# Optimization experiments

Hardware: AMD Instinct MI355X
Metric: run time of the kernel (lower is better)

Reference implementation:

```python
import jax, jax.numpy as jnp
import numpy as np
from jax import lax

B, T, D, H = 32, 512, 1024, 1024


def setup_inputs() -> dict:
    key = jax.random.key(0)
    ks = jax.random.split(key, 6)
    inp = jax.random.normal(ks[0], (B, T, D), jnp.float32)
    attention_mask = jnp.ones((B, T), jnp.float32)
    nonzero_index = jax.random.randint(ks[1], (B, 1), 0, T)
    # Stacked gate weights, gate order (i, f, g, o); equivalent to 8 separate Linears.
    W_x = jax.random.normal(ks[2], (D, 4 * H), jnp.float32) * 0.02
    W_h = jax.random.normal(ks[3], (H, 4 * H), jnp.float32) * 0.02
    b_x = jax.random.normal(ks[4], (4 * H,), jnp.float32) * 0.02
    b_h = jax.random.normal(ks[5], (4 * H,), jnp.float32) * 0.02
    return {"input": inp, "attention_mask": attention_mask, "nonzero_index": nonzero_index,
            "W_x": W_x, "W_h": W_h, "b_x": b_x, "b_h": b_h}


def reference(input, attention_mask, nonzero_index, W_x, W_h, b_x, b_h):
    # Precompute all input-side gate projections in one big matmul: [B,T,4H]
    x_gates = jnp.einsum('btd,dg->btg', input, W_x) + b_x + b_h

    def step(carry, xg):
        h, c = carry                       # [B,H] each
        g = xg + h @ W_h                   # [B,4H]
        i, f, gg, o = jnp.split(g, 4, axis=-1)
        i = jax.nn.sigmoid(i)
        f = jax.nn.sigmoid(f)
        gg = jnp.tanh(gg)
        o = jax.nn.sigmoid(o)
        c = f * c + i * gg
        h = o * jnp.tanh(c)
        return (h, c), (h, c)

    h0 = jnp.zeros((B, H), x_gates.dtype)
    c0 = jnp.zeros((B, H), x_gates.dtype)
    _, (hs, cs) = lax.scan(step, (h0, c0), jnp.swapaxes(x_gates, 0, 1))  # [T,B,H]
    hts = jnp.swapaxes(hs, 0, 1)  # [B,T,H]
    cts = jnp.swapaxes(cs, 0, 1)
    # cls token gathered BEFORE masking (matches original order)
    cls_token = jnp.take_along_axis(hts, nonzero_index[:, :, None], axis=1)[:, 0, :]
    hts = hts * attention_mask[:, :, None]
    cts = cts * attention_mask[:, :, None]
    return (hts, hts, cts, cls_token)
```

## Files before the change

kernel.cpp:

```cpp
#include <hip/hip_runtime.h>
#include <stdint.h>


typedef _Float16 f16;
typedef __attribute__((ext_vector_type(8))) _Float16 f16x8;
typedef __attribute__((ext_vector_type(4))) float f32x4;

#define NG 2
#define BPG 128
#define NW 8

__device__ __forceinline__ float sigm(float v){ return 1.f/(1.f+__expf(-v)); }
__device__ __forceinline__ float tanh_(float v){ return 2.f/(1.f+__expf(-2.f*v)) - 1.f; }

__global__ __launch_bounds__(512, 2) void lstm_kernel(
    const float* __restrict__ xin, const float* __restrict__ amask,
    const int* __restrict__ nzidx, const float* __restrict__ Wx,
    const float* __restrict__ Wh, const float* __restrict__ bx,
    const float* __restrict__ bh, float* __restrict__ out,
    uint32_t* __restrict__ ws)
{
  __shared__ __align__(16) f16 Wl[128][64][8];
  __shared__ __align__(16) float pl[NW][2][64][4];
  __shared__ __align__(16) f16 hstage[16][8];

  const int tid  = threadIdx.x;
  const int lane = tid & 63;
  const int wid  = tid >> 6;
  const int r    = blockIdx.x & 127;
  const int G    = blockIdx.x >> 7;
  const int hbase = r * 8;

  uint32_t* flags = ws + (size_t)G * BPG;
  uint64_t* hb64 = (uint64_t*)(ws + 2 * BPG);

  for (int f = wid; f < 128; f += NW) {
    const int side = f >> 6, kf = (f >> 1) & 31, nt = f & 1;
    const int c16 = lane & 15, kslot = lane >> 4;
    const int g = nt * 2 + (c16 >> 3);
    const int gcol = g * 1024 + hbase + (c16 & 7);
    const int k0 = kf * 32 + kslot * 8;
    const float* Wsrc = side ? Wh : Wx;
    f16x8 v;
#pragma unroll
    for (int e = 0; e < 8; ++e) v[e] = (f16)Wsrc[(size_t)(k0 + e) * 4096 + gcol];
    *(f16x8*)&Wl[f][lane][0] = v;
  }
  const int b  = tid >> 3;
  const int hc = tid & 7;
  const int b_glob = G * 16 + b;
  float bias[4] = {0.f, 0.f, 0.f, 0.f};
  float cval = 0.f;
  int myidx = -1;
  if (tid < 128) {
#pragma unroll
    for (int g = 0; g < 4; ++g) {
      const int gcol = g * 1024 + hbase + hc;
      bias[g] = bx[gcol] + bh[gcol];
    }
    myidx = nzidx[b_glob];
  }
  __syncthreads();

  bool gave_up = false;
#pragma unroll 1
  for (int t = 0; t < 512; ++t) {
    f32x4 acc0 = {0.f,0.f,0.f,0.f}, acc1 = {0.f,0.f,0.f,0.f};
    const int bb = lane & 15, kslot = lane >> 4;
    {
      const size_t xrow = ((size_t)(G * 16 + bb) * 512 + (size_t)t) * 1024;
#pragma unroll
      for (int q = 0; q < 4; ++q) {
        const int kf = wid * 4 + q;
        const int k0 = kf * 32 + kslot * 8;
        const float* xs = xin + xrow + k0;
        f16x8 a;
#pragma unroll
        for (int e = 0; e < 8; ++e) a[e] = (f16)xs[e];
        f16x8 b0 = *(const f16x8*)&Wl[kf * 2 + 0][lane][0];
        f16x8 b1 = *(const f16x8*)&Wl[kf * 2 + 1][lane][0];
        acc0 = __builtin_amdgcn_mfma_f32_16x16x32_f16(a, b0, acc0, 0, 0, 0);
        acc1 = __builtin_amdgcn_mfma_f32_16x16x32_f16(a, b1, acc1, 0, 0, 0);
      }
    }
    if (t > 0) {
      if (!gave_up) {
        const uint32_t tgt = (uint32_t)t;
        int spins = 0;
        for (;;) {
          uint32_t fv = (lane < 16)
            ? __hip_atomic_load(&flags[wid * 16 + lane], __ATOMIC_RELAXED, __HIP_MEMORY_SCOPE_AGENT)
            : tgt;
          if (__all((int)(fv >= tgt))) break;
          if (++spins > (1 << 16)) { gave_up = true; break; }
          __builtin_amdgcn_s_sleep(1);
        }
        __builtin_amdgcn_sched_barrier(0);
      }
      const int p = t & 1;
      const uint64_t* hsrc = hb64 + (size_t)(p * NG + G) * 4096;
#pragma unroll
      for (int q = 0; q < 4; ++q) {
        const int kf = wid * 4 + q;
        const size_t e2 = (size_t)(kf * 64 + lane) * 2;
        uint64_t lo = __hip_atomic_load(hsrc + e2,     __ATOMIC_RELAXED, __HIP_MEMORY_SCOPE_AGENT);
        uint64_t hi = __hip_atomic_load(hsrc + e2 + 1, __ATOMIC_RELAXED, __HIP_MEMORY_SCOPE_AGENT);
        union { uint64_t u[2]; f16x8 v; } cv;
        cv.u[0] = lo; cv.u[1] = hi;
        f16x8 b0 = *(const f16x8*)&Wl[64 + kf * 2 + 0][lane][0];
        f16x8 b1 = *(const f16x8*)&Wl[64 + kf * 2 + 1][lane][0];
        acc0 = __builtin_amdgcn_mfma_f32_16x16x32_f16(cv.v, b0, acc0, 0, 0, 0);
        acc1 = __builtin_amdgcn_mfma_f32_16x16x32_f16(cv.v, b1, acc1, 0, 0, 0);
      }
    }
    *(f32x4*)&pl[wid][0][lane][0] = acc0;
    *(f32x4*)&pl[wid][1][lane][0] = acc1;
    __syncthreads();
    float hval = 0.f, mval = 0.f;
    if (tid < 128) {
      float s[4];
#pragma unroll
      for (int g = 0; g < 4; ++g) {
        const int nt = g >> 1;
        const int lp = ((g & 1) * 8 + hc) + 16 * (b >> 2);
        const int reg = b & 3;
        float v = bias[g];
#pragma unroll
        for (int w = 0; w < NW; ++w) v += pl[w][nt][lp][reg];
        s[g] = v;
      }
      const float ig = sigm(s[0]);
      const float fg = sigm(s[1]);
      const float gg = tanh_(s[2]);
      const float og = sigm(s[3]);
      cval = fg * cval + ig * gg;
      hval = og * tanh_(cval);
      hstage[b][hc] = (f16)hval;
      mval = amask[(size_t)b_glob * 512 + (size_t)t];
    }
    __syncthreads();
    if (wid == 0) {
      if (lane < 32) {
        const int p2 = (t + 1) & 1;
        const uint64_t v = ((const uint64_t*)hstage)[lane];
        const size_t e = (size_t)((r >> 2) * 64 + (r & 3) * 16 + (lane >> 1));
        __hip_atomic_store(hb64 + (size_t)(p2 * NG + G) * 4096 + e * 2 + (lane & 1), v,
                           __ATOMIC_RELAXED, __HIP_MEMORY_SCOPE_AGENT);
      }
      asm volatile("s_waitcnt vmcnt(0)" ::: "memory");
      if (lane == 0)
        __hip_atomic_store(&flags[r], (uint32_t)(t + 1), __ATOMIC_RELAXED, __HIP_MEMORY_SCOPE_AGENT);
    }
    if (tid < 128) {
      const size_t o0 = ((size_t)b_glob * 512 + (size_t)t) * 1024 + (size_t)(hbase + hc);
      out[o0] = hval * mval;
      out[o0 + 16777216u] = hval * mval;
      out[o0 + 33554432u] = cval * mval;
      if (t == myidx) out[50331648u + (size_t)b_glob * 1024 + (size_t)(hbase + hc)] = hval;
    }
  }
}

extern "C" void kernel_launch(void* const* d_in, const int* in_sizes, int n_in,
                              void* d_out, int out_size, void* d_ws, size_t ws_size,
                              hipStream_t stream) {
  const float* xin   = (const float*)d_in[0];
  const float* amask = (const float*)d_in[1];
  const int*   nzidx = (const int*)d_in[2];
  const float* Wx    = (const float*)d_in[3];
  const float* Wh    = (const float*)d_in[4];
  const float* bx    = (const float*)d_in[5];
  const float* bh    = (const float*)d_in[6];
  float* out = (float*)d_out;
  uint32_t* ws = (uint32_t*)d_ws;

  hipMemsetAsync(d_ws, 0, 2 * BPG * sizeof(uint32_t), stream);

  void* args[] = {(void*)&xin, (void*)&amask, (void*)&nzidx, (void*)&Wx,
                  (void*)&Wh, (void*)&bx, (void*)&bh, (void*)&out, (void*)&ws};
  hipError_t e = hipLaunchCooperativeKernel((const void*)lstm_kernel, dim3(256), dim3(512),
                                            args, 0, stream);
  if (e != hipSuccess) {
    lstm_kernel<<<dim3(256), dim3(512), 0, stream>>>(xin, amask, nzidx, Wx, Wh, bx, bh, out, ws);
  }
}
```

Before: 2.158 ms.

## Replicate h broadcast buffers and flags, prefetch x, vectorize weight load and epilogue

Keeps up to 8 replicated copies of the per-step hidden-state buffer and flag arrays, so groups of blocks poll and read separate copies instead of all hitting one location. Hidden-state exchange now uses 16-byte cache-bypassing loads and stores. The x row for the next step is prefetched into registers during the current step, the weight staging uses vector loads, and the gate epilogue runs in a single wave producing two outputs per lane with vectorized stores. It also drops launch_bounds occupancy to 1 and uses more workspace. It risks extra store traffic, and the design depends on the workspace being large enough for the replicas.

```diff
diff --git a/kernel.cpp b/kernel.cpp
--- a/kernel.cpp
+++ b/kernel.cpp
@@ -5,24 +5,34 @@
 typedef _Float16 f16;
 typedef __attribute__((ext_vector_type(8))) _Float16 f16x8;
 typedef __attribute__((ext_vector_type(4))) float f32x4;
+typedef __attribute__((ext_vector_type(4))) unsigned int u32x4;
 
 #define NG 2
 #define BPG 128
 #define NW 8
+#define REPSTRIDE 131072
 
 __device__ __forceinline__ float sigm(float v){ return 1.f/(1.f+__expf(-v)); }
 __device__ __forceinline__ float tanh_(float v){ return 2.f/(1.f+__expf(-2.f*v)) - 1.f; }
 
-__global__ __launch_bounds__(512, 2) void lstm_kernel(
+__device__ __forceinline__ u32x4 ld16_sc(const void* p) {
+  u32x4 r;
+  asm volatile("global_load_dwordx4 %0, %1, off sc0 sc1" : "=v"(r) : "v"(p));
+  return r;
+}
+__device__ __forceinline__ void st16_sc(void* p, u32x4 v) {
+  asm volatile("global_store_dwordx4 %0, %1, off sc0 sc1" :: "v"(p), "v"(v) : "memory");
+}
+
+__global__ __launch_bounds__(512, 1) void lstm_kernel(
     const float* __restrict__ xin, const float* __restrict__ amask,
     const int* __restrict__ nzidx, const float* __restrict__ Wx,
     const float* __restrict__ Wh, const float* __restrict__ bx,
     const float* __restrict__ bh, float* __restrict__ out,
-    uint32_t* __restrict__ ws)
+    uint32_t* __restrict__ ws, int nrep, int flagpg_u32, int h_off_b)
 {
   __shared__ __align__(16) f16 Wl[128][64][8];
   __shared__ __align__(16) float pl[NW][2][64][4];
-  __shared__ __align__(16) f16 hstage[16][8];
 
   const int tid  = threadIdx.x;
   const int lane = tid & 63;
@@ -30,133 +40,175 @@
   const int r    = blockIdx.x & 127;
   const int G    = blockIdx.x >> 7;
   const int hbase = r * 8;
-
-  uint32_t* flags = ws + (size_t)G * BPG;
-  uint64_t* hb64 = (uint64_t*)(ws + 2 * BPG);
-
-  for (int f = wid; f < 128; f += NW) {
-    const int side = f >> 6, kf = (f >> 1) & 31, nt = f & 1;
-    const int c16 = lane & 15, kslot = lane >> 4;
-    const int g = nt * 2 + (c16 >> 3);
-    const int gcol = g * 1024 + hbase + (c16 & 7);
-    const int k0 = kf * 32 + kslot * 8;
-    const float* Wsrc = side ? Wh : Wx;
-    f16x8 v;
-#pragma unroll
-    for (int e = 0; e < 8; ++e) v[e] = (f16)Wsrc[(size_t)(k0 + e) * 4096 + gcol];
-    *(f16x8*)&Wl[f][lane][0] = v;
-  }
-  const int b  = tid >> 3;
-  const int hc = tid & 7;
-  const int b_glob = G * 16 + b;
-  float bias[4] = {0.f, 0.f, 0.f, 0.f};
-  float cval = 0.f;
+  const int rep_c = r & (nrep - 1);
+
+  uint8_t* hb8 = (uint8_t*)ws + h_off_b;
+
+  {
+    const int g = (tid & 7) >> 1, half = tid & 1, row = tid >> 3;
+#pragma unroll 1
+    for (int it = 0; it < 32; ++it) {
+      const int k = it * 64 + row;
+      const int side = k >> 10, kk = k & 1023;
+      const float* Wsrc = side ? Wh : Wx;
+      const f32x4 v = *(const f32x4*)(Wsrc + (size_t)kk * 4096 + g * 1024 + hbase + half * 4);
+      const int f = side * 64 + ((kk >> 5) << 1) + (g >> 1);
+      const int lane0 = (g & 1) * 8 + half * 4 + 16 * ((kk >> 3) & 3);
+      const int e = kk & 7;
+#pragma unroll
+      for (int i = 0; i < 4; ++i) Wl[f][lane0 + i][e] = (f16)v[i];
+    }
+  }
+  const int ob = lane >> 2, ohp = lane & 3;
+  const int b_glob = G * 16 + ob;
+  float bias[4][2];
+  float cv0 = 0.f, cv1 = 0.f;
   int myidx = -1;
-  if (tid < 128) {
+  if (wid == 0) {
 #pragma unroll
     for (int g = 0; g < 4; ++g) {
-      const int gcol = g * 1024 + hbase + hc;
-      bias[g] = bx[gcol] + bh[gcol];
+#pragma unroll
+      for (int j = 0; j < 2; ++j) {
+        const int gcol = g * 1024 + hbase + ohp * 2 + j;
+        bias[g][j] = bx[gcol] + bh[gcol];
+      }
     }
     myidx = nzidx[b_glob];
+  }
+  const int bb = lane & 15, kslot = lane >> 4;
+  f32x4 xf[4][2];
+  {
+    const size_t xrow = ((size_t)(G * 16 + bb) * 512) * 1024;
+#pragma unroll
+    for (int q = 0; q < 4; ++q) {
+      const float* xs = xin + xrow + (wid * 4 + q) * 32 + kslot * 8;
+      xf[q][0] = *(const f32x4*)xs;
+      xf[q][1] = *(const f32x4*)(xs + 4);
+    }
   }
   __syncthreads();
 
   bool gave_up = false;
 #pragma unroll 1
   for (int t = 0; t < 512; ++t) {
+    f16x8 xa[4];
+#pragma unroll
+    for (int q = 0; q < 4; ++q) {
+      f16x8 a;
+#pragma unroll
+      for (int i = 0; i < 4; ++i) { a[i] = (f16)xf[q][0][i]; a[i + 4] = (f16)xf[q][1][i]; }
+      xa[q] = a;
+    }
     f32x4 acc0 = {0.f,0.f,0.f,0.f}, acc1 = {0.f,0.f,0.f,0.f};
-    const int bb = lane & 15, kslot = lane >> 4;
-    {
-      const size_t xrow = ((size_t)(G * 16 + bb) * 512 + (size_t)t) * 1024;
-#pragma unroll
-      for (int q = 0; q < 4; ++q) {
-        const int kf = wid * 4 + q;
-        const int k0 = kf * 32 + kslot * 8;
-        const float* xs = xin + xrow + k0;
-        f16x8 a;
-#pragma unroll
-        for (int e = 0; e < 8; ++e) a[e] = (f16)xs[e];
-        f16x8 b0 = *(const f16x8*)&Wl[kf * 2 + 0][lane][0];
-        f16x8 b1 = *(const f16x8*)&Wl[kf * 2 + 1][lane][0];
-        acc0 = __builtin_amdgcn_mfma_f32_16x16x32_f16(a, b0, acc0, 0, 0, 0);
-        acc1 = __builtin_amdgcn_mfma_f32_16x16x32_f16(a, b1, acc1, 0, 0, 0);
-      }
+#pragma unroll
+    for (int q = 0; q < 4; ++q) {
+      const int kf = wid * 4 + q;
+      f16x8 b0 = *(const f16x8*)&Wl[kf * 2 + 0][lane][0];
+      f16x8 b1 = *(const f16x8*)&Wl[kf * 2 + 1][lane][0];
+      acc0 = __builtin_amdgcn_mfma_f32_16x16x32_f16(xa[q], b0, acc0, 0, 0, 0);
+      acc1 = __builtin_amdgcn_mfma_f32_16x16x32_f16(xa[q], b1, acc1, 0, 0, 0);
     }
     if (t > 0) {
       if (!gave_up) {
         const uint32_t tgt = (uint32_t)t;
+        const uint32_t* fl = ws + (size_t)rep_c * flagpg_u32 + G * BPG + wid * 16;
         int spins = 0;
         for (;;) {
           uint32_t fv = (lane < 16)
-            ? __hip_atomic_load(&flags[wid * 16 + lane], __ATOMIC_RELAXED, __HIP_MEMORY_SCOPE_AGENT)
-            : tgt;
+            ? __hip_atomic_load(fl + lane, __ATOMIC_RELAXED, __HIP_MEMORY_SCOPE_AGENT) : tgt;
           if (__all((int)(fv >= tgt))) break;
           if (++spins > (1 << 16)) { gave_up = true; break; }
           __builtin_amdgcn_s_sleep(1);
         }
         __builtin_amdgcn_sched_barrier(0);
       }
-      const int p = t & 1;
-      const uint64_t* hsrc = hb64 + (size_t)(p * NG + G) * 4096;
+      const uint8_t* hrep = hb8 + (size_t)rep_c * REPSTRIDE + ((size_t)((t & 1) * NG + G) << 15);
+      u32x4 hq[4];
+#pragma unroll
+      for (int q = 0; q < 4; ++q)
+        hq[q] = ld16_sc(hrep + ((size_t)((wid * 4 + q) * 64 + lane) << 4));
+      asm volatile("s_waitcnt vmcnt(0)" ::: "memory");
 #pragma unroll
       for (int q = 0; q < 4; ++q) {
+        union { u32x4 u; f16x8 v; } cv; cv.u = hq[q];
         const int kf = wid * 4 + q;
-        const size_t e2 = (size_t)(kf * 64 + lane) * 2;
-        uint64_t lo = __hip_atomic_load(hsrc + e2,     __ATOMIC_RELAXED, __HIP_MEMORY_SCOPE_AGENT);
-        uint64_t hi = __hip_atomic_load(hsrc + e2 + 1, __ATOMIC_RELAXED, __HIP_MEMORY_SCOPE_AGENT);
-        union { uint64_t u[2]; f16x8 v; } cv;
-        cv.u[0] = lo; cv.u[1] = hi;
         f16x8 b0 = *(const f16x8*)&Wl[64 + kf * 2 + 0][lane][0];
         f16x8 b1 = *(const f16x8*)&Wl[64 + kf * 2 + 1][lane][0];
         acc0 = __builtin_amdgcn_mfma_f32_16x16x32_f16(cv.v, b0, acc0, 0, 0, 0);
         acc1 = __builtin_amdgcn_mfma_f32_16x16x32_f16(cv.v, b1, acc1, 0, 0, 0);
       }
     }
+    if (t + 1 < 512) {
+      const size_t xrow = ((size_t)(G * 16 + bb) * 512 + (size_t)(t + 1)) * 1024;
+#pragma unroll
+      for (int q = 0; q < 4; ++q) {
+        const float* xs = xin + xrow + (wid * 4 + q) * 32 + kslot * 8;
+        xf[q][0] = *(const f32x4*)xs;
+        xf[q][1] = *(const f32x4*)(xs + 4);
+      }
+    }
     *(f32x4*)&pl[wid][0][lane][0] = acc0;
     *(f32x4*)&pl[wid][1][lane][0] = acc1;
     __syncthreads();
-    float hval = 0.f, mval = 0.f;
-    if (tid < 128) {
-      float s[4];
+    float ssum[4][2];
+    if (wid == 0) {
 #pragma unroll
       for (int g = 0; g < 4; ++g) {
-        const int nt = g >> 1;
-        const int lp = ((g & 1) * 8 + hc) + 16 * (b >> 2);
-        const int reg = b & 3;
-        float v = bias[g];
-#pragma unroll
-        for (int w = 0; w < NW; ++w) v += pl[w][nt][lp][reg];
-        s[g] = v;
-      }
-      const float ig = sigm(s[0]);
-      const float fg = sigm(s[1]);
-      const float gg = tanh_(s[2]);
-      const float og = sigm(s[3]);
-      cval = fg * cval + ig * gg;
-      hval = og * tanh_(cval);
-      hstage[b][hc] = (f16)hval;
-      mval = amask[(size_t)b_glob * 512 + (size_t)t];
+#pragma unroll
+        for (int j = 0; j < 2; ++j) {
+          const int lp = (g & 1) * 8 + (ohp * 2 + j) + 16 * (ob >> 2);
+          const int reg = ob & 3;
+          float v = bias[g][j];
+#pragma unroll
+          for (int w = 0; w < NW; ++w) v += pl[w][g >> 1][lp][reg];
+          ssum[g][j] = v;
+        }
+      }
     }
     __syncthreads();
     if (wid == 0) {
-      if (lane < 32) {
-        const int p2 = (t + 1) & 1;
-        const uint64_t v = ((const uint64_t*)hstage)[lane];
-        const size_t e = (size_t)((r >> 2) * 64 + (r & 3) * 16 + (lane >> 1));
-        __hip_atomic_store(hb64 + (size_t)(p2 * NG + G) * 4096 + e * 2 + (lane & 1), v,
-                           __ATOMIC_RELAXED, __HIP_MEMORY_SCOPE_AGENT);
-      }
-      asm volatile("s_waitcnt vmcnt(0)" ::: "memory");
-      if (lane == 0)
-        __hip_atomic_store(&flags[r], (uint32_t)(t + 1), __ATOMIC_RELAXED, __HIP_MEMORY_SCOPE_AGENT);
-    }
-    if (tid < 128) {
-      const size_t o0 = ((size_t)b_glob * 512 + (size_t)t) * 1024 + (size_t)(hbase + hc);
-      out[o0] = hval * mval;
-      out[o0 + 16777216u] = hval * mval;
-      out[o0 + 33554432u] = cval * mval;
-      if (t == myidx) out[50331648u + (size_t)b_glob * 1024 + (size_t)(hbase + hc)] = hval;
+      const float i0 = sigm(ssum[0][0]), i1 = sigm(ssum[0][1]);
+      const float f0 = sigm(ssum[1][0]), f1 = sigm(ssum[1][1]);
+      const float g0 = tanh_(ssum[2][0]), g1 = tanh_(ssum[2][1]);
+      const float o0 = sigm(ssum[3][0]), o1 = sigm(ssum[3][1]);
+      cv0 = f0 * cv0 + i0 * g0;
+      cv1 = f1 * cv1 + i1 * g1;
+      const float hv0 = o0 * tanh_(cv0);
+      const float hv1 = o1 * tanh_(cv1);
+      union { f16 h[2]; uint32_t u; } pk;
+      pk.h[0] = (f16)hv0; pk.h[1] = (f16)hv1;
+      const uint32_t v0 = pk.u;
+      const uint32_t v1 = __shfl_xor((int)v0 * 0 + (int)pk.u, 1, 64);
+      const uint32_t v2 = __shfl_xor((int)pk.u, 2, 64);
+      const uint32_t v3 = __shfl_xor((int)pk.u, 3, 64);
+      const uint32_t t0 = (ohp & 1) ? v1 : v0, t1 = (ohp & 1) ? v0 : v1;
+      const uint32_t t2 = (ohp & 1) ? v3 : v2, t3 = (ohp & 1) ? v2 : v3;
+      u32x4 quad;
+      quad[0] = (ohp & 2) ? t2 : t0; quad[1] = (ohp & 2) ? t3 : t1;
+      quad[2] = (ohp & 2) ? t0 : t2; quad[3] = (ohp & 2) ? t1 : t3;
+      if (t < 511) {
+        const size_t unit = (size_t)((r >> 2) * 64 + ob + 16 * (r & 3)) << 4;
+        const size_t poff = (size_t)(((t + 1) & 1) * NG + G) << 15;
+        if (ohp < nrep)
+          st16_sc(hb8 + (size_t)ohp * REPSTRIDE + poff + unit, quad);
+        if (ohp + 4 < nrep)
+          st16_sc(hb8 + (size_t)(ohp + 4) * REPSTRIDE + poff + unit, quad);
+        asm volatile("s_waitcnt vmcnt(0)" ::: "memory");
+        if (lane < nrep)
+          __hip_atomic_store(ws + (size_t)lane * flagpg_u32 + G * BPG + r, (uint32_t)(t + 1),
+                             __ATOMIC_RELAXED, __HIP_MEMORY_SCOPE_AGENT);
+      }
+      const float mval = amask[(size_t)b_glob * 512 + (size_t)t];
+      const size_t o0p = ((size_t)b_glob * 512 + (size_t)t) * 1024 + (size_t)(hbase + ohp * 2);
+      const float2 hm = {hv0 * mval, hv1 * mval};
+      const float2 cm = {cv0 * mval, cv1 * mval};
+      *(float2*)(out + o0p) = hm;
+      *(float2*)(out + o0p + 16777216u) = hm;
+      *(float2*)(out + o0p + 33554432u) = cm;
+      if (t == myidx) {
+        const float2 hr = {hv0, hv1};
+        *(float2*)(out + 50331648u + (size_t)b_glob * 1024 + (size_t)(hbase + ohp * 2)) = hr;
+      }
     }
   }
 }
@@ -174,13 +226,21 @@
   float* out = (float*)d_out;
   uint32_t* ws = (uint32_t*)d_ws;
 
-  hipMemsetAsync(d_ws, 0, 2 * BPG * sizeof(uint32_t), stream);
+  size_t flagpg = 4096; int nrep = 8;
+  while (nrep > 1 && ws_size < (size_t)nrep * (flagpg + REPSTRIDE)) nrep >>= 1;
+  if (ws_size < flagpg + REPSTRIDE) flagpg = 1024;
+  int flagpg_u32 = (int)(flagpg / 4);
+  int h_off_b = (int)((size_t)nrep * flagpg);
+
+  hipMemsetAsync(d_ws, 0, (size_t)nrep * flagpg, stream);
 
   void* args[] = {(void*)&xin, (void*)&amask, (void*)&nzidx, (void*)&Wx,
-                  (void*)&Wh, (void*)&bx, (void*)&bh, (void*)&out, (void*)&ws};
+                  (void*)&Wh, (void*)&bx, (void*)&bh, (void*)&out, (void*)&ws,
+                  (void*)&nrep, (void*)&flagpg_u32, (void*)&h_off_b};
   hipError_t e = hipLaunchCooperativeKernel((const void*)lstm_kernel, dim3(256), dim3(512),
                                             args, 0, stream);
   if (e != hipSuccess) {
-    lstm_kernel<<<dim3(256), dim3(512), 0, stream>>>(xin, amask, nzidx, Wx, Wh, bx, bh, out, ws);
-  }
-}
+    lstm_kernel<<<dim3(256), dim3(512), 0, stream>>>(xin, amask, nzidx, Wx, Wh, bx, bh,
+                                                     out, ws, nrep, flagpg_u32, h_off_b);
+  }
+}
```

After: 2.969 ms. +37.6%, slower.

## Embed step tags in h exchange packets and prefetch next x row

Applied to the files above, without the earlier changes.

Replaces the separate per-block flag array with a timestamp stored inside each 16-byte h packet. Consumers spin directly on the data loads with cache-bypassing sc0 sc1 accesses until every packet carries the current step, which removes the flag round trip and the ordering wait between data and flag stores. The input row for step t+1 is loaded into registers while step t computes, hiding global load latency. Packets double in size, the whole exchange buffer must be zeroed each launch, and launch bounds drop to one block per CU.

```diff
diff --git a/kernel.cpp b/kernel.cpp
--- a/kernel.cpp
+++ b/kernel.cpp
@@ -5,15 +5,25 @@
 typedef _Float16 f16;
 typedef __attribute__((ext_vector_type(8))) _Float16 f16x8;
 typedef __attribute__((ext_vector_type(4))) float f32x4;
+typedef __attribute__((ext_vector_type(4))) unsigned int u32x4;
 
 #define NG 2
-#define BPG 128
 #define NW 8
+#define HBYTES (2 * NG * 2048 * 32)
 
 __device__ __forceinline__ float sigm(float v){ return 1.f/(1.f+__expf(-v)); }
 __device__ __forceinline__ float tanh_(float v){ return 2.f/(1.f+__expf(-2.f*v)) - 1.f; }
 
-__global__ __launch_bounds__(512, 2) void lstm_kernel(
+__device__ __forceinline__ u32x4 ld16_sc(const void* p) {
+  u32x4 r;
+  asm volatile("global_load_dwordx4 %0, %1, off sc0 sc1" : "=v"(r) : "v"(p));
+  return r;
+}
+__device__ __forceinline__ void st16_sc(void* p, u32x4 v) {
+  asm volatile("global_store_dwordx4 %0, %1, off sc0 sc1" :: "v"(p), "v"(v) : "memory");
+}
+
+__global__ __launch_bounds__(512, 1) void lstm_kernel(
     const float* __restrict__ xin, const float* __restrict__ amask,
     const int* __restrict__ nzidx, const float* __restrict__ Wx,
     const float* __restrict__ Wh, const float* __restrict__ bx,
@@ -31,8 +41,7 @@
   const int G    = blockIdx.x >> 7;
   const int hbase = r * 8;
 
-  uint32_t* flags = ws + (size_t)G * BPG;
-  uint64_t* hb64 = (uint64_t*)(ws + 2 * BPG);
+  uint8_t* hb8 = (uint8_t*)ws;
 
   for (int f = wid; f < 128; f += NW) {
     const int side = f >> 6, kf = (f >> 1) & 31, nt = f & 1;
@@ -60,57 +69,82 @@
     }
     myidx = nzidx[b_glob];
   }
+  const int bb = lane & 15, kslot = lane >> 4;
+  f32x4 xf[4][2];
+  {
+    const size_t xrow = ((size_t)(G * 16 + bb) * 512) * 1024;
+#pragma unroll
+    for (int q = 0; q < 4; ++q) {
+      const float* xs = xin + xrow + (wid * 4 + q) * 32 + kslot * 8;
+      xf[q][0] = *(const f32x4*)xs;
+      xf[q][1] = *(const f32x4*)(xs + 4);
+    }
+  }
   __syncthreads();
 
   bool gave_up = false;
 #pragma unroll 1
   for (int t = 0; t < 512; ++t) {
+    f16x8 xa[4];
+#pragma unroll
+    for (int q = 0; q < 4; ++q) {
+      f16x8 a;
+#pragma unroll
+      for (int i = 0; i < 4; ++i) { a[i] = (f16)xf[q][0][i]; a[i + 4] = (f16)xf[q][1][i]; }
+      xa[q] = a;
+    }
     f32x4 acc0 = {0.f,0.f,0.f,0.f}, acc1 = {0.f,0.f,0.f,0.f};
-    const int bb = lane & 15, kslot = lane >> 4;
-    {
-      const size_t xrow = ((size_t)(G * 16 + bb) * 512 + (size_t)t) * 1024;
+#pragma unroll
+    for (int q = 0; q < 4; ++q) {
+      const int kf = wid * 4 + q;
+      f16x8 b0 = *(const f16x8*)&Wl[kf * 2 + 0][lane][0];
+      f16x8 b1 = *(const f16x8*)&Wl[kf * 2 + 1][lane][0];
+      acc0 = __builtin_amdgcn_mfma_f32_16x16x32_f16(xa[q], b0, acc0, 0, 0, 0);
+      acc1 = __builtin_amdgcn_mfma_f32_16x16x32_f16(xa[q], b1, acc1, 0, 0, 0);
+    }
+    if (t > 0) {
+      const uint8_t* hsrc = hb8 + ((size_t)((t & 1) * NG + G) << 16);
+      u32x4 ha[4], hbq[4];
+      int spins = 0;
+      for (;;) {
+#pragma unroll
+        for (int q = 0; q < 4; ++q) {
+          const uint8_t* up = hsrc + (((size_t)(wid * 4 + q) * 64 + lane) << 5);
+          ha[q]  = ld16_sc(up);
+          hbq[q] = ld16_sc(up + 16);
+        }
+        asm volatile("s_waitcnt vmcnt(0)" ::: "memory");
+        if (gave_up) break;
+        uint32_t tmin = ha[0][2];
+#pragma unroll
+        for (int q = 0; q < 4; ++q) {
+          tmin = tmin < ha[q][2]  ? tmin : ha[q][2];
+          tmin = tmin < hbq[q][2] ? tmin : hbq[q][2];
+        }
+        if (__all((int)(tmin >= (uint32_t)t))) break;
+        if (++spins > (1 << 13)) { gave_up = true; break; }
+        __builtin_amdgcn_s_sleep(1);
+      }
+      __builtin_amdgcn_sched_barrier(0);
 #pragma unroll
       for (int q = 0; q < 4; ++q) {
+        union { u32x4 u; f16x8 v; } cv;
+        cv.u[0] = ha[q][0]; cv.u[1] = ha[q][1];
+        cv.u[2] = hbq[q][0]; cv.u[3] = hbq[q][1];
         const int kf = wid * 4 + q;
-        const int k0 = kf * 32 + kslot * 8;
-        const float* xs = xin + xrow + k0;
-        f16x8 a;
-#pragma unroll
-        for (int e = 0; e < 8; ++e) a[e] = (f16)xs[e];
-        f16x8 b0 = *(const f16x8*)&Wl[kf * 2 + 0][lane][0];
-        f16x8 b1 = *(const f16x8*)&Wl[kf * 2 + 1][lane][0];
-        acc0 = __builtin_amdgcn_mfma_f32_16x16x32_f16(a, b0, acc0, 0, 0, 0);
-        acc1 = __builtin_amdgcn_mfma_f32_16x16x32_f16(a, b1, acc1, 0, 0, 0);
-      }
-    }
-    if (t > 0) {
-      if (!gave_up) {
-        const uint32_t tgt = (uint32_t)t;
-        int spins = 0;
-        for (;;) {
-          uint32_t fv = (lane < 16)
-            ? __hip_atomic_load(&flags[wid * 16 + lane], __ATOMIC_RELAXED, __HIP_MEMORY_SCOPE_AGENT)
-            : tgt;
-          if (__all((int)(fv >= tgt))) break;
-          if (++spins > (1 << 16)) { gave_up = true; break; }
-          __builtin_amdgcn_s_sleep(1);
-        }
-        __builtin_amdgcn_sched_barrier(0);
-      }
-      const int p = t & 1;
-      const uint64_t* hsrc = hb64 + (size_t)(p * NG + G) * 4096;
-#pragma unroll
-      for (int q = 0; q < 4; ++q) {
-        const int kf = wid * 4 + q;
-        const size_t e2 = (size_t)(kf * 64 + lane) * 2;
-        uint64_t lo = __hip_atomic_load(hsrc + e2,     __ATOMIC_RELAXED, __HIP_MEMORY_SCOPE_AGENT);
-        uint64_t hi = __hip_atomic_load(hsrc + e2 + 1, __ATOMIC_RELAXED, __HIP_MEMORY_SCOPE_AGENT);
-        union { uint64_t u[2]; f16x8 v; } cv;
-        cv.u[0] = lo; cv.u[1] = hi;
         f16x8 b0 = *(const f16x8*)&Wl[64 + kf * 2 + 0][lane][0];
         f16x8 b1 = *(const f16x8*)&Wl[64 + kf * 2 + 1][lane][0];
         acc0 = __builtin_amdgcn_mfma_f32_16x16x32_f16(cv.v, b0, acc0, 0, 0, 0);
         acc1 = __builtin_amdgcn_mfma_f32_16x16x32_f16(cv.v, b1, acc1, 0, 0, 0);
+      }
+    }
+    if (t + 1 < 512) {
+      const size_t xrow = ((size_t)(G * 16 + bb) * 512 + (size_t)(t + 1)) * 1024;
+#pragma unroll
+      for (int q = 0; q < 4; ++q) {
+        const float* xs = xin + xrow + (wid * 4 + q) * 32 + kslot * 8;
+        xf[q][0] = *(const f32x4*)xs;
+        xf[q][1] = *(const f32x4*)(xs + 4);
       }
     }
     *(f32x4*)&pl[wid][0][lane][0] = acc0;
@@ -121,12 +155,11 @@
       float s[4];
 #pragma unroll
       for (int g = 0; g < 4; ++g) {
-        const int nt = g >> 1;
         const int lp = ((g & 1) * 8 + hc) + 16 * (b >> 2);
         const int reg = b & 3;
         float v = bias[g];
 #pragma unroll
-        for (int w = 0; w < NW; ++w) v += pl[w][nt][lp][reg];
+        for (int w = 0; w < NW; ++w) v += pl[w][g >> 1][lp][reg];
         s[g] = v;
       }
       const float ig = sigm(s[0]);
@@ -139,17 +172,14 @@
       mval = amask[(size_t)b_glob * 512 + (size_t)t];
     }
     __syncthreads();
-    if (wid == 0) {
-      if (lane < 32) {
-        const int p2 = (t + 1) & 1;
-        const uint64_t v = ((const uint64_t*)hstage)[lane];
-        const size_t e = (size_t)((r >> 2) * 64 + (r & 3) * 16 + (lane >> 1));
-        __hip_atomic_store(hb64 + (size_t)(p2 * NG + G) * 4096 + e * 2 + (lane & 1), v,
-                           __ATOMIC_RELAXED, __HIP_MEMORY_SCOPE_AGENT);
-      }
-      asm volatile("s_waitcnt vmcnt(0)" ::: "memory");
-      if (lane == 0)
-        __hip_atomic_store(&flags[r], (uint32_t)(t + 1), __ATOMIC_RELAXED, __HIP_MEMORY_SCOPE_AGENT);
+    if (wid == 0 && lane < 32 && t < 511) {
+      const int ob = lane >> 1, half = lane & 1;
+      const uint32_t* hrow = (const uint32_t*)&hstage[ob][half * 4];
+      u32x4 q;
+      q[0] = hrow[0]; q[1] = hrow[1]; q[2] = (uint32_t)(t + 1); q[3] = 0u;
+      const size_t unit = (size_t)((r >> 2) * 64 + (r & 3) * 16 + ob);
+      uint8_t* dst = hb8 + ((size_t)(((t + 1) & 1) * NG + G) << 16) + unit * 32 + half * 16;
+      st16_sc(dst, q);
     }
     if (tid < 128) {
       const size_t o0 = ((size_t)b_glob * 512 + (size_t)t) * 1024 + (size_t)(hbase + hc);
@@ -174,7 +204,7 @@
   float* out = (float*)d_out;
   uint32_t* ws = (uint32_t*)d_ws;
 
-  hipMemsetAsync(d_ws, 0, 2 * BPG * sizeof(uint32_t), stream);
+  hipMemsetAsync(d_ws, 0, HBYTES, stream);
 
   void* args[] = {(void*)&xin, (void*)&amask, (void*)&nzidx, (void*)&Wx,
                   (void*)&Wh, (void*)&bx, (void*)&bh, (void*)&out, (void*)&ws};
```

Result: slower. 2.461 ms (+14.0%).
